# Performance work log

Measured on AMD Instinct MI355X. Metric: run time of the kernel, lower is better.

Reference implementation:

```python
import jax, jax.numpy as jnp
import numpy as np

D_MODEL, D_LOW, NUM_BINS = 512, 64, 39
DIST_MIN, DIST_MAX = 2.0, 22.0
BIN_WIDTH = (DIST_MAX - DIST_MIN) / (NUM_BINS - 1)
LN_EPS = 1e-5


def setup_inputs() -> dict:
    key = jax.random.key(0)
    ks = jax.random.split(key, 10)
    B, N = 2, 768
    h_res = jax.random.normal(ks[0], (B, N, D_MODEL), dtype=jnp.float32)
    # scale coords so pairwise distances span the [2, 22] bin range
    x_true = jax.random.normal(ks[1], (B, N, 3), dtype=jnp.float32) * 5.0
    token_pad_mask = jnp.ones((B, N), dtype=jnp.float32)
    s = 1.0 / np.sqrt(D_MODEL)
    return {
        "h_res": h_res,
        "x_true": x_true,
        "token_pad_mask": token_pad_mask,
        "ln_w": jnp.ones((D_MODEL,), jnp.float32),
        "ln_b": jnp.zeros((D_MODEL,), jnp.float32),
        "wu_w": jax.random.normal(ks[2], (D_LOW, D_MODEL), jnp.float32) * s,
        "wu_b": jnp.zeros((D_LOW,), jnp.float32),
        "wv_w": jax.random.normal(ks[3], (D_LOW, D_MODEL), jnp.float32) * s,
        "wv_b": jnp.zeros((D_LOW,), jnp.float32),
        "wb_w": jax.random.normal(ks[4], (NUM_BINS, D_LOW), jnp.float32) * (1.0 / np.sqrt(D_LOW)),
        "wb_b": jnp.zeros((NUM_BINS,), jnp.float32),
    }


def _layernorm(x, w, b):
    mu = jnp.mean(x, axis=-1, keepdims=True)
    var = jnp.mean(jnp.square(x - mu), axis=-1, keepdims=True)
    return (x - mu) * jax.lax.rsqrt(var + LN_EPS) * w + b


def reference(h_res, x_true, token_pad_mask, ln_w, ln_b, wu_w, wu_b, wv_w, wv_b, wb_w, wb_b):
    B, N, _ = h_res.shape
    # pairwise distances -> target bins (trunc-to-int then clamp, as torch .long())
    diff = x_true[:, :, None, :] - x_true[:, None, :, :]          # [B,N,N,3]
    d_true = jnp.sqrt(jnp.sum(diff * diff, axis=-1))               # [B,N,N]
    target = jnp.clip(((d_true - DIST_MIN) / BIN_WIDTH).astype(jnp.int32), 0, NUM_BINS - 1)

    h = _layernorm(h_res, ln_w, ln_b)
    U = h @ wu_w.T + wu_b                                          # [B,N,d_low]
    V = h @ wv_w.T + wv_b                                          # [B,N,d_low]
    # logits[b,i,j,k] = sum_c U[b,i,c] V[b,j,c] Wb[k,c] + bb[k]
    logits = jnp.einsum("bic,bjc,kc->bijk", U, V, wb_w) + wb_b     # [B,N,N,K]
    logp = jax.nn.log_softmax(logits, axis=-1)
    ce = -jnp.take_along_axis(logp, target[..., None], axis=-1)[..., 0]  # [B,N,N]

    mask = (token_pad_mask[:, :, None] * token_pad_mask[:, None, :]) > 0  # [B,N,N] bool
    counts = jnp.sum(mask, axis=(1, 2))                            # [B]
    per_sample = jnp.sum(jnp.where(mask, ce, 0.0), axis=(1, 2)) / jnp.maximum(counts, 1)
    valid = counts > 0
    total_count = jnp.sum(valid)
    loss = jnp.sum(jnp.where(valid, per_sample, 0.0)) / jnp.maximum(total_count, 1)
    return loss
```

## Files before the change

### kernel.cpp

```cpp
#include <hip/hip_runtime.h>
#include <hip/hip_bf16.h>
#include <math.h>

#define D_MODEL 512
#define D_LOW   64
#define NBINS   39
#define LOG2E   1.4426950408889634f
#define LN2     0.6931471805599453f

typedef __attribute__((ext_vector_type(8))) short short8;
typedef __attribute__((ext_vector_type(4))) float floatx4;

__global__ __launch_bounds__(256) void prep_kernel(
    const float* __restrict__ ln_w, const float* __restrict__ ln_b,
    const float* __restrict__ wu_w, const float* __restrict__ wu_b,
    const float* __restrict__ wv_w, const float* __restrict__ wv_b,
    __hip_bfloat16* __restrict__ w2bf, float* __restrict__ w2sum,
    float* __restrict__ b2) {
  __shared__ float red[8];
  const int tid = threadIdx.x;
  const int o = blockIdx.x;
  const bool isU = (o < 64);
  const float* wrow = isU ? (wu_w + o * D_MODEL) : (wv_w + (o - 64) * D_MODEL);
  const float scale = isU ? LOG2E : 1.0f;

  float s1 = 0.f, s2 = 0.f;
  #pragma unroll
  for (int cc = 0; cc < 2; ++cc) {
    const int c = tid + cc * 256;
    const float w  = wrow[c];
    const float w2 = w * ln_w[c] * scale;
    const __hip_bfloat16 hb = __float2bfloat16(w2);
    w2bf[o * D_MODEL + c] = hb;
    s1 += __bfloat162float(hb);
    s2 += w * ln_b[c];
  }
  #pragma unroll
  for (int off = 32; off; off >>= 1) {
    s1 += __shfl_xor(s1, off);
    s2 += __shfl_xor(s2, off);
  }
  const int wave = tid >> 6, lane = tid & 63;
  if (lane == 0) { red[wave] = s1; red[4 + wave] = s2; }
  __syncthreads();
  if (tid == 0) {
    w2sum[o] = red[0] + red[1] + red[2] + red[3];
    const float ss2 = red[4] + red[5] + red[6] + red[7];
    b2[o] = scale * ((isU ? wu_b[o] : wv_b[o - 64]) + ss2);
  }
}

__global__ __launch_bounds__(64) void lnproj_kernel(
    const float* __restrict__ h_res, const __hip_bfloat16* __restrict__ w2bf,
    const float* __restrict__ w2sum, const float* __restrict__ b2,
    float* __restrict__ U, __hip_bfloat16* __restrict__ Vbf, int N) {
  const int lane = threadIdx.x;
  const int q = lane >> 4, ln16 = lane & 15;
  const int rt = blockIdx.x >> 3, og = blockIdx.x & 7;
  const int row0 = rt * 16;
  const float* hp = h_res + (size_t)(row0 + ln16) * D_MODEL + q * 8;

  short8 abf[16];
  float sum = 0.f, ssq = 0.f;
  #pragma unroll
  for (int kc = 0; kc < 16; ++kc) {
    const floatx4 x0 = *reinterpret_cast<const floatx4*>(hp + kc * 32);
    const floatx4 x1 = *reinterpret_cast<const floatx4*>(hp + kc * 32 + 4);
    short8 a;
    #pragma unroll
    for (int e = 0; e < 4; ++e) {
      sum += x0[e]; ssq += x0[e] * x0[e];
      const __hip_bfloat16 hb = __float2bfloat16(x0[e]);
      a[e] = *reinterpret_cast<const short*>(&hb);
    }
    #pragma unroll
    for (int e = 0; e < 4; ++e) {
      sum += x1[e]; ssq += x1[e] * x1[e];
      const __hip_bfloat16 hb = __float2bfloat16(x1[e]);
      a[4 + e] = *reinterpret_cast<const short*>(&hb);
    }
    abf[kc] = a;
  }
  sum += __shfl_xor(sum, 16); sum += __shfl_xor(sum, 32);
  ssq += __shfl_xor(ssq, 16); ssq += __shfl_xor(ssq, 32);
  const float mu  = sum * (1.0f / (float)D_MODEL);
  const float var = ssq * (1.0f / (float)D_MODEL) - mu * mu;
  const float rs  = rsqrtf(var + 1e-5f);
  float mu_r[4], rs_r[4];
  #pragma unroll
  for (int r = 0; r < 4; ++r) {
    mu_r[r] = __shfl(mu, q * 4 + r);
    rs_r[r] = __shfl(rs, q * 4 + r);
  }

  const int out = og * 16 + ln16;
  const short* wp = reinterpret_cast<const short*>(w2bf);
  floatx4 acc = (floatx4){0.f, 0.f, 0.f, 0.f};
  #pragma unroll
  for (int kc = 0; kc < 16; ++kc) {
    const short8 bfr = *reinterpret_cast<const short8*>(
        wp + (size_t)out * D_MODEL + kc * 32 + q * 8);
    acc = __builtin_amdgcn_mfma_f32_16x16x32_bf16(abf[kc], bfr, acc, 0, 0, 0);
  }

  const float ws = w2sum[out];
  const float bb = b2[out];
  #pragma unroll
  for (int r = 0; r < 4; ++r) {
    const int rowg = row0 + q * 4 + r;
    const float val = rs_r[r] * acc[r] - mu_r[r] * rs_r[r] * ws + bb;
    if (out < 64) {
      U[(size_t)rowg * D_LOW + out] = val;
    } else {
      Vbf[(size_t)rowg * D_LOW + (out - 64)] = __float2bfloat16(val);
    }
  }
}

__global__ __launch_bounds__(256) void wprep_kernel(
    const float* __restrict__ U, const float* __restrict__ wb_w,
    short* __restrict__ wfragbuf, int BN) {
  __shared__ float wsh[NBINS * 65];
  const int tid = threadIdx.x;
  for (int e = tid; e < NBINS * D_LOW; e += 256) {
    const int n = e >> 6, c = e & 63;
    wsh[n * 65 + c] = wb_w[e];
  }
  __syncthreads();

  const int wave = tid >> 6, lane = tid & 63;
  const int q = lane >> 4, ln16 = lane & 15;
  const int rowi = blockIdx.x * 4 + wave;
  const float* Up = U + (size_t)rowi * D_LOW;

  float u[16];
  #pragma unroll
  for (int s = 0; s < 2; ++s)
    #pragma unroll
    for (int e = 0; e < 8; ++e) u[s * 8 + e] = Up[s * 32 + q * 8 + e];

  short* outp = wfragbuf + (size_t)rowi * 6 * 64 * 8;
  #pragma unroll
  for (int t = 0; t < 3; ++t) {
    const int n = t * 16 + ln16;
    #pragma unroll
    for (int s = 0; s < 2; ++s) {
      short8 f;
      #pragma unroll
      for (int e = 0; e < 8; ++e) {
        const float w = (n < NBINS) ? wsh[n * 65 + s * 32 + q * 8 + e] : 0.f;
        const float v = u[s * 8 + e] * w;
        const __hip_bfloat16 hb = __float2bfloat16(v);
        f[e] = *reinterpret_cast<const short*>(&hb);
      }
      *reinterpret_cast<short8*>(outp + ((size_t)(t * 2 + s) * 64 + lane) * 8) = f;
    }
  }
}

__global__ __launch_bounds__(256) void pair_kernel(
    const short* __restrict__ wfragbuf,
    const __hip_bfloat16* __restrict__ Vbf,
    const float* __restrict__ wb_b,
    const float* __restrict__ x_true, const float* __restrict__ pmask,
    float* __restrict__ part, int N) {
  __shared__ float rbuf[8];
  const int i    = blockIdx.x;
  const int b    = blockIdx.y >> 2;
  const int qtr  = blockIdx.y & 3;
  const int tid  = threadIdx.x;
  const int wave = tid >> 6, lane = tid & 63;
  const int q = lane >> 4, ln16 = lane & 15;
  const int rowi = b * N + i;
  const int jbase = qtr * (N >> 2) + wave * (N >> 4);
  const int q4 = q * 4;

  short8 wfrag[3][2];
  {
    const short* wfp = wfragbuf + (size_t)rowi * 6 * 64 * 8;
    #pragma unroll
    for (int t = 0; t < 3; ++t)
      #pragma unroll
      for (int s = 0; s < 2; ++s)
        wfrag[t][s] = *reinterpret_cast<const short8*>(
            wfp + ((size_t)(t * 2 + s) * 64 + lane) * 8);
  }

  const short* Vp = reinterpret_cast<const short*>(Vbf) + (size_t)b * N * D_LOW;
  short8 v[3][2];
  #pragma unroll
  for (int tl = 0; tl < 3; ++tl) {
    const size_t jr = jbase + tl * 16 + ln16;
    v[tl][0] = *reinterpret_cast<const short8*>(Vp + jr * D_LOW + q * 8);
    v[tl][1] = *reinterpret_cast<const short8*>(Vp + jr * D_LOW + 32 + q * 8);
  }

  const float xi0 = x_true[rowi * 3 + 0];
  const float xi1 = x_true[rowi * 3 + 1];
  const float xi2 = x_true[rowi * 3 + 2];
  const float pmi = pmask[rowi];
  const float BW  = (22.0f - 2.0f) / 38.0f;
  int tbv[3];
  #pragma unroll
  for (int tl = 0; tl < 3; ++tl) {
    const int rowj = b * N + jbase + tl * 16 + ln16;
    const float dx = xi0 - x_true[rowj * 3 + 0];
    const float dy = xi1 - x_true[rowj * 3 + 1];
    const float dz = xi2 - x_true[rowj * 3 + 2];
    const float d  = sqrtf(dx * dx + dy * dy + dz * dz);
    int tb = (int)((d - 2.0f) / BW);
    tb = tb < 0 ? 0 : (tb > NBINS - 1 ? NBINS - 1 : tb);
    tbv[tl] = (pmi * pmask[rowj] > 0.f) ? tb : -1;
  }

  floatx4 bias_init[3];
  #pragma unroll
  for (int t = 0; t < 3; ++t)
    #pragma unroll
    for (int r = 0; r < 4; ++r) {
      const int bin = t * 16 + q * 4 + r;
      bias_init[t][r] = (bin < NBINS) ? LOG2E * wb_b[bin] : -INFINITY;
    }

  float ce_sum = 0.f, cnt_sum = 0.f;
  #pragma unroll
  for (int tl = 0; tl < 3; ++tl) {
    floatx4 f[3];
    #pragma unroll
    for (int t = 0; t < 3; ++t) {
      floatx4 a = bias_init[t];
      a = __builtin_amdgcn_mfma_f32_16x16x32_bf16(wfrag[t][0], v[tl][0], a, 0, 0, 0);
      a = __builtin_amdgcn_mfma_f32_16x16x32_bf16(wfrag[t][1], v[tl][1], a, 0, 0, 0);
      f[t] = a;
    }

    const int tb  = tbv[tl];
    const int tbq = tb - q4;
    float s0 = 0.f, s1 = 0.f, s2 = 0.f, s3 = 0.f, lt = 0.f;
    #pragma unroll
    for (int t = 0; t < 3; ++t) {
      const floatx4 fv = f[t];
      s0 += __builtin_amdgcn_exp2f(fv[0]);
      s1 += __builtin_amdgcn_exp2f(fv[1]);
      s2 += __builtin_amdgcn_exp2f(fv[2]);
      s3 += __builtin_amdgcn_exp2f(fv[3]);
      lt += (tbq == t * 16 + 0) ? fv[0] : 0.f;
      lt += (tbq == t * 16 + 1) ? fv[1] : 0.f;
      lt += (tbq == t * 16 + 2) ? fv[2] : 0.f;
      lt += (tbq == t * 16 + 3) ? fv[3] : 0.f;
    }
    float ssum = (s0 + s1) + (s2 + s3);
    ssum += __shfl_xor(ssum, 16); ssum += __shfl_xor(ssum, 32);
    const float ok = (tb >= 0) ? 1.f : 0.f;
    ce_sum  += ok * LN2 * (__builtin_amdgcn_logf(ssum) - 4.0f * lt);
    cnt_sum += ok;
  }

  #pragma unroll
  for (int off = 32; off; off >>= 1) {
    ce_sum  += __shfl_xor(ce_sum, off);
    cnt_sum += __shfl_xor(cnt_sum, off);
  }
  if (lane == 0) { rbuf[wave] = ce_sum; rbuf[4 + wave] = cnt_sum; }
  __syncthreads();
  if (tid == 0) {
    const size_t slot = ((size_t)blockIdx.y * N + blockIdx.x) * 2;
    part[slot + 0] = rbuf[0] + rbuf[1] + rbuf[2] + rbuf[3];
    part[slot + 1] = rbuf[4] + rbuf[5] + rbuf[6] + rbuf[7];
  }
}

__global__ __launch_bounds__(256) void finalize_kernel(
    const float* __restrict__ part, float* __restrict__ out, int N, int B) {
  __shared__ float red[8];
  const int tid = threadIdx.x, wave = tid >> 6, lane = tid & 63;
  float loss = 0.f, vcount = 0.f;
  const int nper = 4 * N;
  for (int b = 0; b < B; ++b) {
    float ce = 0.f, cnt = 0.f;
    for (int e = tid; e < nper; e += 256) {
      const size_t base = ((size_t)b * nper + e) * 2;
      ce  += part[base + 0];
      cnt += part[base + 1];
    }
    #pragma unroll
    for (int off = 32; off; off >>= 1) {
      ce  += __shfl_xor(ce, off);
      cnt += __shfl_xor(cnt, off);
    }
    if (lane == 0) { red[wave] = ce; red[4 + wave] = cnt; }
    __syncthreads();
    if (tid == 0) {
      const float s = red[0] + red[1] + red[2] + red[3];
      const float c = red[4] + red[5] + red[6] + red[7];
      if (c > 0.f) { loss += s / fmaxf(c, 1.f); vcount += 1.f; }
    }
    __syncthreads();
  }
  if (tid == 0) out[0] = (vcount > 0.f) ? loss / vcount : 0.f;
}

extern "C" void kernel_launch(void* const* d_in, const int* in_sizes, int n_in,
                              void* d_out, int out_size, void* d_ws, size_t ws_size,
                              hipStream_t stream) {
  const float* h_res  = (const float*)d_in[0];
  const float* x_true = (const float*)d_in[1];
  const float* pmask  = (const float*)d_in[2];
  const float* ln_w   = (const float*)d_in[3];
  const float* ln_b   = (const float*)d_in[4];
  const float* wu_w   = (const float*)d_in[5];
  const float* wu_b   = (const float*)d_in[6];
  const float* wv_w   = (const float*)d_in[7];
  const float* wv_b   = (const float*)d_in[8];
  const float* wb_w   = (const float*)d_in[9];
  const float* wb_b   = (const float*)d_in[10];

  const int B  = 2;
  const int N  = in_sizes[2] / B;
  const int BN = B * N;

  float* U = (float*)d_ws;
  __hip_bfloat16* Vbf = (__hip_bfloat16*)(U + (size_t)BN * D_LOW);
  float* part = (float*)(Vbf + (size_t)BN * D_LOW);
  __hip_bfloat16* w2bf = (__hip_bfloat16*)(part + (size_t)8 * N * 2);
  float* w2sum = (float*)(w2bf + 128 * D_MODEL);
  float* b2    = w2sum + 128;
  short* wfragbuf = (short*)(b2 + 128);

  prep_kernel<<<128, 256, 0, stream>>>(ln_w, ln_b, wu_w, wu_b, wv_w, wv_b,
                                       w2bf, w2sum, b2);
  lnproj_kernel<<<(BN / 16) * 8, 64, 0, stream>>>(h_res, w2bf, w2sum, b2,
                                                  U, Vbf, N);
  wprep_kernel<<<BN / 4, 256, 0, stream>>>(U, wb_w, wfragbuf, BN);
  pair_kernel<<<dim3(N, 4 * B), 256, 0, stream>>>(
      wfragbuf, Vbf, wb_b, x_true, pmask, part, N);
  finalize_kernel<<<1, 256, 0, stream>>>(part, (float*)d_out, N, B);
}
```

Measured before the change: 132.0 us.

## Fuse wfrag prep into pair kernel, share h_res across outputs in lnproj

Removes the separate wprep kernel and its global wfrag buffer, building the U*Wb bf16 fragments in LDS at the start of each pair block. lnproj now has one 512-thread block per 16 rows, so h_res is read once into LDS instead of once per output group, with the LayerNorm statistics reduced across waves. The pair kernel handles twice as many j per block (6 tiles per wave, half of N per block), which amortises the fragment build but halves the grid. This saves a launch and a round trip through global memory, at the cost of repeating the fragment computation in every block and having fewer blocks.

Result: faster. 124.5 us (-5.7%).

```diff
diff --git a/kernel.cpp b/kernel.cpp
--- a/kernel.cpp
+++ b/kernel.cpp
@@ -50,22 +50,24 @@
   }
 }
 
-__global__ __launch_bounds__(64) void lnproj_kernel(
+__global__ __launch_bounds__(512) void lnproj_kernel(
     const float* __restrict__ h_res, const __hip_bfloat16* __restrict__ w2bf,
     const float* __restrict__ w2sum, const float* __restrict__ b2,
     float* __restrict__ U, __hip_bfloat16* __restrict__ Vbf, int N) {
-  const int lane = threadIdx.x;
+  __shared__ short abuf[16 * 512];
+  __shared__ float sred[8][2][16];
+  const int tid = threadIdx.x;
+  const int wv = tid >> 6, lane = tid & 63;
   const int q = lane >> 4, ln16 = lane & 15;
-  const int rt = blockIdx.x >> 3, og = blockIdx.x & 7;
-  const int row0 = rt * 16;
-  const float* hp = h_res + (size_t)(row0 + ln16) * D_MODEL + q * 8;
-
-  short8 abf[16];
+  const int row0 = blockIdx.x * 16;
+
   float sum = 0.f, ssq = 0.f;
   #pragma unroll
-  for (int kc = 0; kc < 16; ++kc) {
-    const floatx4 x0 = *reinterpret_cast<const floatx4*>(hp + kc * 32);
-    const floatx4 x1 = *reinterpret_cast<const floatx4*>(hp + kc * 32 + 4);
+  for (int k2 = 0; k2 < 2; ++k2) {
+    const int kc = wv * 2 + k2;
+    const float* hp = h_res + (size_t)(row0 + ln16) * D_MODEL + kc * 32 + q * 8;
+    const floatx4 x0 = *reinterpret_cast<const floatx4*>(hp);
+    const floatx4 x1 = *reinterpret_cast<const floatx4*>(hp + 4);
     short8 a;
     #pragma unroll
     for (int e = 0; e < 4; ++e) {
@@ -79,28 +81,36 @@
       const __hip_bfloat16 hb = __float2bfloat16(x1[e]);
       a[4 + e] = *reinterpret_cast<const short*>(&hb);
     }
-    abf[kc] = a;
+    *reinterpret_cast<short8*>(&abuf[kc * 512 + q * 128 + ln16 * 8]) = a;
   }
   sum += __shfl_xor(sum, 16); sum += __shfl_xor(sum, 32);
   ssq += __shfl_xor(ssq, 16); ssq += __shfl_xor(ssq, 32);
-  const float mu  = sum * (1.0f / (float)D_MODEL);
-  const float var = ssq * (1.0f / (float)D_MODEL) - mu * mu;
-  const float rs  = rsqrtf(var + 1e-5f);
+  if (lane < 16) { sred[wv][0][ln16] = sum; sred[wv][1][ln16] = ssq; }
+  __syncthreads();
+
   float mu_r[4], rs_r[4];
   #pragma unroll
   for (int r = 0; r < 4; ++r) {
-    mu_r[r] = __shfl(mu, q * 4 + r);
-    rs_r[r] = __shfl(rs, q * 4 + r);
-  }
-
-  const int out = og * 16 + ln16;
+    const int row = q * 4 + r;
+    float s = 0.f, s2 = 0.f;
+    #pragma unroll
+    for (int w = 0; w < 8; ++w) { s += sred[w][0][row]; s2 += sred[w][1][row]; }
+    const float mu  = s * (1.0f / (float)D_MODEL);
+    const float var = s2 * (1.0f / (float)D_MODEL) - mu * mu;
+    mu_r[r] = mu;
+    rs_r[r] = rsqrtf(var + 1e-5f);
+  }
+
+  const int out = wv * 16 + ln16;
   const short* wp = reinterpret_cast<const short*>(w2bf);
   floatx4 acc = (floatx4){0.f, 0.f, 0.f, 0.f};
   #pragma unroll
   for (int kc = 0; kc < 16; ++kc) {
+    const short8 afr = *reinterpret_cast<const short8*>(
+        &abuf[kc * 512 + q * 128 + ln16 * 8]);
     const short8 bfr = *reinterpret_cast<const short8*>(
         wp + (size_t)out * D_MODEL + kc * 32 + q * 8);
-    acc = __builtin_amdgcn_mfma_f32_16x16x32_bf16(abf[kc], bfr, acc, 0, 0, 0);
+    acc = __builtin_amdgcn_mfma_f32_16x16x32_bf16(afr, bfr, acc, 0, 0, 0);
   }
 
   const float ws = w2sum[out];
@@ -117,82 +127,54 @@
   }
 }
 
-__global__ __launch_bounds__(256) void wprep_kernel(
-    const float* __restrict__ U, const float* __restrict__ wb_w,
-    short* __restrict__ wfragbuf, int BN) {
-  __shared__ float wsh[NBINS * 65];
-  const int tid = threadIdx.x;
-  for (int e = tid; e < NBINS * D_LOW; e += 256) {
-    const int n = e >> 6, c = e & 63;
-    wsh[n * 65 + c] = wb_w[e];
-  }
-  __syncthreads();
-
-  const int wave = tid >> 6, lane = tid & 63;
-  const int q = lane >> 4, ln16 = lane & 15;
-  const int rowi = blockIdx.x * 4 + wave;
-  const float* Up = U + (size_t)rowi * D_LOW;
-
-  float u[16];
-  #pragma unroll
-  for (int s = 0; s < 2; ++s)
-    #pragma unroll
-    for (int e = 0; e < 8; ++e) u[s * 8 + e] = Up[s * 32 + q * 8 + e];
-
-  short* outp = wfragbuf + (size_t)rowi * 6 * 64 * 8;
-  #pragma unroll
-  for (int t = 0; t < 3; ++t) {
-    const int n = t * 16 + ln16;
-    #pragma unroll
-    for (int s = 0; s < 2; ++s) {
-      short8 f;
-      #pragma unroll
-      for (int e = 0; e < 8; ++e) {
-        const float w = (n < NBINS) ? wsh[n * 65 + s * 32 + q * 8 + e] : 0.f;
-        const float v = u[s * 8 + e] * w;
-        const __hip_bfloat16 hb = __float2bfloat16(v);
-        f[e] = *reinterpret_cast<const short*>(&hb);
-      }
-      *reinterpret_cast<short8*>(outp + ((size_t)(t * 2 + s) * 64 + lane) * 8) = f;
-    }
-  }
-}
-
 __global__ __launch_bounds__(256) void pair_kernel(
-    const short* __restrict__ wfragbuf,
-    const __hip_bfloat16* __restrict__ Vbf,
-    const float* __restrict__ wb_b,
+    const float* __restrict__ U, const __hip_bfloat16* __restrict__ Vbf,
+    const float* __restrict__ wb_w, const float* __restrict__ wb_b,
     const float* __restrict__ x_true, const float* __restrict__ pmask,
     float* __restrict__ part, int N) {
+  __shared__ short wsh[6 * 64 * 8];
   __shared__ float rbuf[8];
   const int i    = blockIdx.x;
-  const int b    = blockIdx.y >> 2;
-  const int qtr  = blockIdx.y & 3;
+  const int b    = blockIdx.y >> 1;
+  const int half = blockIdx.y & 1;
   const int tid  = threadIdx.x;
   const int wave = tid >> 6, lane = tid & 63;
   const int q = lane >> 4, ln16 = lane & 15;
   const int rowi = b * N + i;
-  const int jbase = qtr * (N >> 2) + wave * (N >> 4);
+  const int jbase = half * (N >> 1) + wave * (N >> 3);
   const int q4 = q * 4;
 
-  short8 wfrag[3][2];
-  {
-    const short* wfp = wfragbuf + (size_t)rowi * 6 * 64 * 8;
-    #pragma unroll
-    for (int t = 0; t < 3; ++t)
-      #pragma unroll
-      for (int s = 0; s < 2; ++s)
-        wfrag[t][s] = *reinterpret_cast<const short8*>(
-            wfp + ((size_t)(t * 2 + s) * 64 + lane) * 8);
-  }
-
   const short* Vp = reinterpret_cast<const short*>(Vbf) + (size_t)b * N * D_LOW;
-  short8 v[3][2];
-  #pragma unroll
-  for (int tl = 0; tl < 3; ++tl) {
+  short8 v[6][2];
+  #pragma unroll
+  for (int tl = 0; tl < 6; ++tl) {
     const size_t jr = jbase + tl * 16 + ln16;
     v[tl][0] = *reinterpret_cast<const short8*>(Vp + jr * D_LOW + q * 8);
     v[tl][1] = *reinterpret_cast<const short8*>(Vp + jr * D_LOW + 32 + q * 8);
+  }
+
+  for (int slot = tid; slot < 384; slot += 256) {
+    const int fidx = slot >> 6, l = slot & 63;
+    const int t = fidx >> 1, s = fidx & 1;
+    const int lq = l >> 4, l16 = l & 15;
+    const int n = t * 16 + l16;
+    short8 fr = (short8){0, 0, 0, 0, 0, 0, 0, 0};
+    if (n < NBINS) {
+      const float* up = U + (size_t)rowi * D_LOW + s * 32 + lq * 8;
+      const float* wr = wb_w + (size_t)n * D_LOW + s * 32 + lq * 8;
+      const floatx4 u0 = *reinterpret_cast<const floatx4*>(up);
+      const floatx4 u1 = *reinterpret_cast<const floatx4*>(up + 4);
+      const floatx4 w0 = *reinterpret_cast<const floatx4*>(wr);
+      const floatx4 w1 = *reinterpret_cast<const floatx4*>(wr + 4);
+      #pragma unroll
+      for (int e = 0; e < 4; ++e) {
+        const __hip_bfloat16 h0 = __float2bfloat16(u0[e] * w0[e]);
+        const __hip_bfloat16 h1 = __float2bfloat16(u1[e] * w1[e]);
+        fr[e]     = *reinterpret_cast<const short*>(&h0);
+        fr[4 + e] = *reinterpret_cast<const short*>(&h1);
+      }
+    }
+    *reinterpret_cast<short8*>(&wsh[slot * 8]) = fr;
   }
 
   const float xi0 = x_true[rowi * 3 + 0];
@@ -200,9 +182,9 @@
   const float xi2 = x_true[rowi * 3 + 2];
   const float pmi = pmask[rowi];
   const float BW  = (22.0f - 2.0f) / 38.0f;
-  int tbv[3];
-  #pragma unroll
-  for (int tl = 0; tl < 3; ++tl) {
+  int tbv[6];
+  #pragma unroll
+  for (int tl = 0; tl < 6; ++tl) {
     const int rowj = b * N + jbase + tl * 16 + ln16;
     const float dx = xi0 - x_true[rowj * 3 + 0];
     const float dy = xi1 - x_true[rowj * 3 + 1];
@@ -222,9 +204,18 @@
       bias_init[t][r] = (bin < NBINS) ? LOG2E * wb_b[bin] : -INFINITY;
     }
 
+  __syncthreads();
+  short8 wfrag[3][2];
+  #pragma unroll
+  for (int t = 0; t < 3; ++t)
+    #pragma unroll
+    for (int s = 0; s < 2; ++s)
+      wfrag[t][s] = *reinterpret_cast<const short8*>(
+          &wsh[((t * 2 + s) * 64 + lane) * 8]);
+
   float ce_sum = 0.f, cnt_sum = 0.f;
   #pragma unroll
-  for (int tl = 0; tl < 3; ++tl) {
+  for (int tl = 0; tl < 6; ++tl) {
     floatx4 f[3];
     #pragma unroll
     for (int t = 0; t < 3; ++t) {
@@ -275,7 +266,7 @@
   __shared__ float red[8];
   const int tid = threadIdx.x, wave = tid >> 6, lane = tid & 63;
   float loss = 0.f, vcount = 0.f;
-  const int nper = 4 * N;
+  const int nper = 2 * N;
   for (int b = 0; b < B; ++b) {
     float ce = 0.f, cnt = 0.f;
     for (int e = tid; e < nper; e += 256) {
@@ -322,17 +313,15 @@
   float* U = (float*)d_ws;
   __hip_bfloat16* Vbf = (__hip_bfloat16*)(U + (size_t)BN * D_LOW);
   float* part = (float*)(Vbf + (size_t)BN * D_LOW);
-  __hip_bfloat16* w2bf = (__hip_bfloat16*)(part + (size_t)8 * N * 2);
+  __hip_bfloat16* w2bf = (__hip_bfloat16*)(part + (size_t)2 * B * N * 2);
   float* w2sum = (float*)(w2bf + 128 * D_MODEL);
   float* b2    = w2sum + 128;
-  short* wfragbuf = (short*)(b2 + 128);
 
   prep_kernel<<<128, 256, 0, stream>>>(ln_w, ln_b, wu_w, wu_b, wv_w, wv_b,
                                        w2bf, w2sum, b2);
-  lnproj_kernel<<<(BN / 16) * 8, 64, 0, stream>>>(h_res, w2bf, w2sum, b2,
-                                                  U, Vbf, N);
-  wprep_kernel<<<BN / 4, 256, 0, stream>>>(U, wb_w, wfragbuf, BN);
-  pair_kernel<<<dim3(N, 4 * B), 256, 0, stream>>>(
-      wfragbuf, Vbf, wb_b, x_true, pmask, part, N);
+  lnproj_kernel<<<BN / 16, 512, 0, stream>>>(h_res, w2bf, w2sum, b2,
+                                             U, Vbf, N);
+  pair_kernel<<<dim3(N, 2 * B), 256, 0, stream>>>(
+      U, Vbf, wb_w, wb_b, x_true, pmask, part, N);
   finalize_kernel<<<1, 256, 0, stream>>>(part, (float*)d_out, N, B);
 }
```
